# Performance work log

Measured on AMD Instinct MI355X. Metric: run time of the kernel, lower is better.

The kernel has to match this reference:

```python
import jax, jax.numpy as jnp
import numpy as np

INPUT_DIM = 512
MIX = 32
HID = 96
B, T = 256, 512


def setup_inputs() -> dict:
    key = jax.random.key(0)
    ks = jax.random.split(key, 8)
    s = lambda fan_in: 1.0 / np.sqrt(fan_in)
    x = jax.random.normal(ks[0], (B, T, INPUT_DIM), dtype=jnp.float32)
    # mix: Linear(INPUT_DIM, MIX, bias=False) -> weight [MIX, INPUT_DIM]
    W_mix = jax.random.uniform(ks[1], (MIX, INPUT_DIM), jnp.float32, -s(INPUT_DIM), s(INPUT_DIM))
    # GRU layer 0 weights, PyTorch layout: [3H, in], [3H, H], biases [3H]
    W_ih = jax.random.uniform(ks[2], (3 * HID, MIX), jnp.float32, -s(HID), s(HID))
    W_hh = jax.random.uniform(ks[3], (3 * HID, HID), jnp.float32, -s(HID), s(HID))
    b_ih = jax.random.uniform(ks[4], (3 * HID,), jnp.float32, -s(HID), s(HID))
    b_hh = jax.random.uniform(ks[5], (3 * HID,), jnp.float32, -s(HID), s(HID))
    # head: Linear(HID, MIX)
    W_head = jax.random.uniform(ks[6], (MIX, HID), jnp.float32, -s(HID), s(HID))
    b_head = jax.random.uniform(ks[7], (MIX,), jnp.float32, -s(HID), s(HID))
    return {"x": x, "W_mix": W_mix, "W_ih": W_ih, "W_hh": W_hh,
            "b_ih": b_ih, "b_hh": b_hh, "W_head": W_head, "b_head": b_head}


def _gru_last(z, W_ih, W_hh, b_ih, b_hh):
    # z: [B, T, MIX]. Precompute all input-side gate pre-activations: [T, B, 3H]
    gx = jnp.einsum('btm,gm->tbg', z, W_ih) + b_ih
    h0 = jnp.zeros((z.shape[0], HID), dtype=z.dtype)

    def step(h, gx_t):
        gh = h @ W_hh.T + b_hh  # [B, 3H]
        xr, xz, xn = jnp.split(gx_t, 3, axis=-1)
        hr, hz, hn = jnp.split(gh, 3, axis=-1)
        r = jax.nn.sigmoid(xr + hr)
        u = jax.nn.sigmoid(xz + hz)
        n = jnp.tanh(xn + r * hn)
        h_new = (1.0 - u) * n + u * h
        return h_new, None

    h_last, _ = jax.lax.scan(step, h0, gx)
    return h_last  # [B, HID]


def reference(x, W_mix, W_ih, W_hh, b_ih, b_hh, W_head, b_head):
    z = x @ W_mix.T                       # [B, T, MIX]
    last = _gru_last(z, W_ih, W_hh, b_ih, b_hh)  # [B, HID]
    z_next = last @ W_head.T + b_head     # [B, MIX]
    y_next = z_next @ W_mix               # [B, INPUT_DIM] (tied weights)
    return y_next
```

## Files before the change

### kernel.cpp

```cpp
#include <hip/hip_runtime.h>

#define IDIM 512
#define MIXD 32
#define HID 96
#define BB 256
#define TT 512
#define TROWS 32
#define SROW 516

typedef float f32x2 __attribute__((ext_vector_type(2)));
typedef float f32x4 __attribute__((ext_vector_type(4)));

#define EXP2(x) __builtin_amdgcn_exp2f(x)

template <int CTRL>
__device__ __forceinline__ float dpp_shl_add(float x) {
    int m = __builtin_amdgcn_update_dpp(0, __float_as_int(x), CTRL, 0xf, 0xf, true);
    return x + __int_as_float(m);
}
__device__ __forceinline__ float octet_reduce_lane0(float x) {
    x = dpp_shl_add<0x104>(x);
    x = dpp_shl_add<0x102>(x);
    x = dpp_shl_add<0x101>(x);
    return x;
}
__device__ __forceinline__ float red16(float x) {
    x = dpp_shl_add<0x108>(x);
    x = dpp_shl_add<0x104>(x);
    x = dpp_shl_add<0x102>(x);
    x = dpp_shl_add<0x101>(x);
    return x;
}
__device__ __forceinline__ f32x2 pkfma(f32x2 a, f32x2 b, f32x2 c) {
    asm("v_pk_fma_f32 %0, %1, %2, %0" : "+v"(c) : "v"(a), "v"(b));
    return c;
}

__global__ __launch_bounds__(256) void k_mix(const float* __restrict__ x,
                                             const float* __restrict__ Wmix,
                                             float* __restrict__ z) {
    __shared__ __align__(16) float sx[TROWS * SROW];
    const int tid = threadIdx.x;
    const int mg = (tid >> 4) & 7, ks = tid & 15, rr = tid >> 7;

    f32x2 w[4][16];
    #pragma unroll
    for (int mm = 0; mm < 4; ++mm) {
        #pragma unroll
        for (int i = 0; i < 8; ++i) {
            const int cj = (i + ks) & 7;
            f32x4 v = *(const f32x4*)(Wmix + (size_t)(4 * mg + mm) * IDIM + ks * 32 + cj * 4);
            w[mm][2*i] = v.xy; w[mm][2*i+1] = v.zw;
        }
    }

    const size_t rowbase = (size_t)blockIdx.x * 256;
    const float* xb = x + rowbase * IDIM;

    f32x4 st[16];
    #pragma unroll
    for (int i = 0; i < 16; ++i)
        st[i] = *(const f32x4*)(xb + (size_t)(tid + 256 * i) * 4);

    for (int t = 0; t < 8; ++t) {
        #pragma unroll
        for (int i = 0; i < 16; ++i) {
            const int v = tid + 256 * i, r = v >> 7, c = v & 127;
            *(f32x4*)(&sx[r * SROW + c * 4]) = st[i];
        }
        __syncthreads();

        if (t + 1 < 8) {
            const float* xn = xb + (size_t)(t + 1) * TROWS * IDIM;
            #pragma unroll
            for (int i = 0; i < 16; ++i)
                st[i] = *(const f32x4*)(xn + (size_t)(tid + 256 * i) * 4);
        }

        float* zp = z + (rowbase + (size_t)t * TROWS) * MIXD + 4 * mg;
        for (int rl = 0; rl < 16; ++rl) {
            const int r = rr * 16 + rl;
            const float* rp = sx + r * SROW + ks * 32;
            f32x2 a0 = {0.f,0.f}, a1 = {0.f,0.f}, a2 = {0.f,0.f}, a3 = {0.f,0.f};
            #pragma unroll
            for (int i = 0; i < 8; ++i) {
                f32x4 v = *(const f32x4*)(rp + ((i + ks) & 7) * 4);
                a0 = pkfma(w[0][2*i], v.xy, a0); a0 = pkfma(w[0][2*i+1], v.zw, a0);
                a1 = pkfma(w[1][2*i], v.xy, a1); a1 = pkfma(w[1][2*i+1], v.zw, a1);
                a2 = pkfma(w[2][2*i], v.xy, a2); a2 = pkfma(w[2][2*i+1], v.zw, a2);
                a3 = pkfma(w[3][2*i], v.xy, a3); a3 = pkfma(w[3][2*i+1], v.zw, a3);
            }
            float s0 = red16(a0.x + a0.y);
            float s1 = red16(a1.x + a1.y);
            float s2 = red16(a2.x + a2.y);
            float s3 = red16(a3.x + a3.y);
            if (ks == 0) {
                f32x4 o4 = { s0, s1, s2, s3 };
                *(f32x4*)(zp + (size_t)r * MIXD) = o4;
            }
        }
        __syncthreads();
    }
}

__global__ __launch_bounds__(256, 1) void k_scan(const float* __restrict__ z,
                                                 const float* __restrict__ Wih,
                                                 const float* __restrict__ Whh,
                                                 const float* __restrict__ bih,
                                                 const float* __restrict__ bhh,
                                                 const float* __restrict__ Whead,
                                                 const float* __restrict__ bhead,
                                                 const float* __restrict__ Wmix,
                                                 float* __restrict__ y) {
    const int b   = blockIdx.x;
    const int tid = threadIdx.x;
    const int j0  = tid >> 3;
    const int o   = tid & 7;
    const float L  = 1.4426950408889634f;
    const float L2 = 2.8853900817779268f;

    __shared__ __align__(16) float sz[256 * MIXD];
    __shared__ __align__(16) float shp[2][HID];
    __shared__ __align__(16) float szn[MIXD];

    f32x2 whr[3][6], whu[3][6], whn[3][6], wir[3][2], wiu[3][2], win[3][2];
    float br[3], bu[3], bxn[3], bhn[3];
    #pragma unroll
    for (int i = 0; i < 3; ++i) {
        const int j = j0 + 32 * i;
        #pragma unroll
        for (int c = 0; c < 3; ++c) {
            f32x4 v = *(const f32x4*)(Whh + (size_t)(j        ) * HID + o * 12 + c * 4);
            v *= L;  whr[i][2*c] = v.xy; whr[i][2*c+1] = v.zw;
        }
        #pragma unroll
        for (int c = 0; c < 3; ++c) {
            f32x4 v = *(const f32x4*)(Whh + (size_t)(j +   HID) * HID + o * 12 + c * 4);
            v *= L;  whu[i][2*c] = v.xy; whu[i][2*c+1] = v.zw;
        }
        #pragma unroll
        for (int c = 0; c < 3; ++c) {
            f32x4 v = *(const f32x4*)(Whh + (size_t)(j + 2*HID) * HID + o * 12 + c * 4);
            v *= L2; whn[i][2*c] = v.xy; whn[i][2*c+1] = v.zw;
        }
        {
            f32x4 v = *(const f32x4*)(Wih + (size_t)(j        ) * MIXD + o * 4);
            v *= L;  wir[i][0] = v.xy; wir[i][1] = v.zw;
        }
        {
            f32x4 v = *(const f32x4*)(Wih + (size_t)(j +   HID) * MIXD + o * 4);
            v *= L;  wiu[i][0] = v.xy; wiu[i][1] = v.zw;
        }
        {
            f32x4 v = *(const f32x4*)(Wih + (size_t)(j + 2*HID) * MIXD + o * 4);
            v *= L2; win[i][0] = v.xy; win[i][1] = v.zw;
        }
        br[i]  = (o == 0) ? L  * (bih[j]       + bhh[j])       : 0.f;
        bu[i]  = (o == 0) ? L  * (bih[j + HID] + bhh[j + HID]) : 0.f;
        bxn[i] = (o == 0) ? L2 * bih[j + 2*HID] : 0.f;
        bhn[i] = (o == 0) ? L2 * bhh[j + 2*HID] : 0.f;
    }

    float hown[3] = {0.f, 0.f, 0.f};
    if (tid < HID) shp[0][tid] = 0.f;

    const f32x4* zb4 = (const f32x4*)(z + (size_t)b * TT * MIXD);
    f32x4* sz4 = (f32x4*)sz;

    for (int c = 0; c < TT / 256; ++c) {
        #pragma unroll
        for (int i = 0; i < 8; ++i)
            sz4[tid + 256 * i] = zb4[c * 2048 + tid + 256 * i];
        __syncthreads();

        for (int tt = 0; tt < 256; ++tt) {
            const int t = (c << 8) + tt;
            const float* hr = shp[t & 1];
            float*       hw = shp[(t + 1) & 1];

            const f32x4 z4 = *(const f32x4*)(sz + tt * MIXD + o * 4);
            const f32x4 h0 = *(const f32x4*)(hr + o * 12);
            const f32x4 h1 = *(const f32x4*)(hr + o * 12 + 4);
            const f32x4 h2 = *(const f32x4*)(hr + o * 12 + 8);
            const f32x2 hh[6] = { h0.xy, h0.zw, h1.xy, h1.zw, h2.xy, h2.zw };

            float hv[3];
            #pragma unroll
            for (int i = 0; i < 3; ++i) {
                f32x2 aR  = {br[i],  0.f}, aU  = {bu[i],  0.f};
                f32x2 aXN = {bxn[i], 0.f}, aHN = {bhn[i], 0.f};

                aR  = __builtin_elementwise_fma(wir[i][0], z4.xy, aR);
                aR  = __builtin_elementwise_fma(wir[i][1], z4.zw, aR);
                aU  = __builtin_elementwise_fma(wiu[i][0], z4.xy, aU);
                aU  = __builtin_elementwise_fma(wiu[i][1], z4.zw, aU);
                aXN = __builtin_elementwise_fma(win[i][0], z4.xy, aXN);
                aXN = __builtin_elementwise_fma(win[i][1], z4.zw, aXN);

                #pragma unroll
                for (int k = 0; k < 6; ++k) {
                    aR  = __builtin_elementwise_fma(whr[i][k], hh[k], aR);
                    aU  = __builtin_elementwise_fma(whu[i][k], hh[k], aU);
                    aHN = __builtin_elementwise_fma(whn[i][k], hh[k], aHN);
                }

                float sR  = octet_reduce_lane0(aR.x  + aR.y);
                float sU  = octet_reduce_lane0(aU.x  + aU.y);
                float sXN = octet_reduce_lane0(aXN.x + aXN.y);
                float sHN = octet_reduce_lane0(aHN.x + aHN.y);

                float r = __builtin_amdgcn_rcpf(1.f + EXP2(-sR));
                float u = __builtin_amdgcn_rcpf(1.f + EXP2(-sU));
                float n = 1.f - 2.f * __builtin_amdgcn_rcpf(1.f + EXP2(sXN + r * sHN));
                hv[i] = u * (hown[i] - n) + n;
                hown[i] = hv[i];
            }
            if (o == 0) {
                hw[j0]      = hv[0];
                hw[j0 + 32] = hv[1];
                hw[j0 + 64] = hv[2];
            }
            __syncthreads();
        }
    }

    if (tid < MIXD) {
        const float* h = shp[0];
        float a0 = 0.f, a1 = 0.f, a2 = 0.f, a3 = 0.f;
        #pragma unroll
        for (int kc = 0; kc < HID / 4; ++kc) {
            f32x4 wv = *(const f32x4*)(Whead + (size_t)tid * HID + kc * 4);
            f32x4 hv4 = *(const f32x4*)(h + kc * 4);
            a0 += wv.x * hv4.x; a1 += wv.y * hv4.y;
            a2 += wv.z * hv4.z; a3 += wv.w * hv4.w;
        }
        szn[tid] = bhead[tid] + ((a0 + a1) + (a2 + a3));
    }
    __syncthreads();
    #pragma unroll
    for (int rep = 0; rep < 2; ++rep) {
        const int col = tid + 256 * rep;
        float acc = 0.f;
        #pragma unroll
        for (int m = 0; m < MIXD; ++m)
            acc += szn[m] * Wmix[(size_t)m * IDIM + col];
        y[(size_t)b * IDIM + col] = acc;
    }
}

extern "C" void kernel_launch(void* const* d_in, const int* in_sizes, int n_in,
                              void* d_out, int out_size, void* d_ws, size_t ws_size,
                              hipStream_t stream) {
    const float* x     = (const float*)d_in[0];
    const float* Wmix  = (const float*)d_in[1];
    const float* Wih   = (const float*)d_in[2];
    const float* Whh   = (const float*)d_in[3];
    const float* bih   = (const float*)d_in[4];
    const float* bhh   = (const float*)d_in[5];
    const float* Whead = (const float*)d_in[6];
    const float* bhead = (const float*)d_in[7];
    float* out = (float*)d_out;

    float* z = (float*)d_ws;

    k_mix <<<512, 256, 0, stream>>>(x, Wmix, z);
    k_scan<<<BB,  256, 0, stream>>>(z, Wih, Whh, bih, bhh, Whead, bhead, Wmix, out);
}
```

Before: 328.7 us.

## Pack two batch sequences per block in the GRU scan kernel

The scan kernel now runs 512-thread blocks, with each 256-thread half handling its own batch row. The grid is halved to 128 blocks, and shared buffers for z, the hidden state and the head output are duplicated per half. The aim is to interleave two independent recurrences on one CU so each hides the other's per-step latency. In exchange, both sequences share every block-wide barrier and only half as many CUs are busy. The 512-thread launch bound may also tighten the register budget for the large per-thread weight cache and cause spills.

```diff
diff --git a/kernel.cpp b/kernel.cpp
--- a/kernel.cpp
+++ b/kernel.cpp
@@ -103,7 +103,7 @@
     }
 }
 
-__global__ __launch_bounds__(256, 1) void k_scan(const float* __restrict__ z,
+__global__ __launch_bounds__(512, 1) void k_scan(const float* __restrict__ z,
                                                  const float* __restrict__ Wih,
                                                  const float* __restrict__ Whh,
                                                  const float* __restrict__ bih,
@@ -112,16 +112,18 @@
                                                  const float* __restrict__ bhead,
                                                  const float* __restrict__ Wmix,
                                                  float* __restrict__ y) {
-    const int b   = blockIdx.x;
-    const int tid = threadIdx.x;
-    const int j0  = tid >> 3;
-    const int o   = tid & 7;
+    const int tid  = threadIdx.x;
+    const int half = tid >> 8;
+    const int t2   = tid & 255;
+    const int b    = blockIdx.x * 2 + half;
+    const int j0   = t2 >> 3;
+    const int o    = t2 & 7;
     const float L  = 1.4426950408889634f;
     const float L2 = 2.8853900817779268f;
 
-    __shared__ __align__(16) float sz[256 * MIXD];
-    __shared__ __align__(16) float shp[2][HID];
-    __shared__ __align__(16) float szn[MIXD];
+    __shared__ __align__(16) float sz[2][256 * MIXD];
+    __shared__ __align__(16) float shp[2][2][HID];
+    __shared__ __align__(16) float szn[2][MIXD];
 
     f32x2 whr[3][6], whu[3][6], whn[3][6], wir[3][2], wiu[3][2], win[3][2];
     float br[3], bu[3], bxn[3], bhn[3];
@@ -162,23 +164,23 @@
     }
 
     float hown[3] = {0.f, 0.f, 0.f};
-    if (tid < HID) shp[0][tid] = 0.f;
+    if (t2 < HID) shp[half][0][t2] = 0.f;
 
     const f32x4* zb4 = (const f32x4*)(z + (size_t)b * TT * MIXD);
-    f32x4* sz4 = (f32x4*)sz;
+    f32x4* sz4 = (f32x4*)sz[half];
 
     for (int c = 0; c < TT / 256; ++c) {
         #pragma unroll
         for (int i = 0; i < 8; ++i)
-            sz4[tid + 256 * i] = zb4[c * 2048 + tid + 256 * i];
+            sz4[t2 + 256 * i] = zb4[c * 2048 + t2 + 256 * i];
         __syncthreads();
 
         for (int tt = 0; tt < 256; ++tt) {
             const int t = (c << 8) + tt;
-            const float* hr = shp[t & 1];
-            float*       hw = shp[(t + 1) & 1];
-
-            const f32x4 z4 = *(const f32x4*)(sz + tt * MIXD + o * 4);
+            const float* hr = shp[half][t & 1];
+            float*       hw = shp[half][(t + 1) & 1];
+
+            const f32x4 z4 = *(const f32x4*)(sz[half] + tt * MIXD + o * 4);
             const f32x4 h0 = *(const f32x4*)(hr + o * 12);
             const f32x4 h1 = *(const f32x4*)(hr + o * 12 + 4);
             const f32x4 h2 = *(const f32x4*)(hr + o * 12 + 8);
@@ -224,26 +226,26 @@
         }
     }
 
-    if (tid < MIXD) {
-        const float* h = shp[0];
+    if (t2 < MIXD) {
+        const float* h = shp[half][0];
         float a0 = 0.f, a1 = 0.f, a2 = 0.f, a3 = 0.f;
         #pragma unroll
         for (int kc = 0; kc < HID / 4; ++kc) {
-            f32x4 wv = *(const f32x4*)(Whead + (size_t)tid * HID + kc * 4);
+            f32x4 wv = *(const f32x4*)(Whead + (size_t)t2 * HID + kc * 4);
             f32x4 hv4 = *(const f32x4*)(h + kc * 4);
             a0 += wv.x * hv4.x; a1 += wv.y * hv4.y;
             a2 += wv.z * hv4.z; a3 += wv.w * hv4.w;
         }
-        szn[tid] = bhead[tid] + ((a0 + a1) + (a2 + a3));
+        szn[half][t2] = bhead[t2] + ((a0 + a1) + (a2 + a3));
     }
     __syncthreads();
     #pragma unroll
     for (int rep = 0; rep < 2; ++rep) {
-        const int col = tid + 256 * rep;
+        const int col = t2 + 256 * rep;
         float acc = 0.f;
         #pragma unroll
         for (int m = 0; m < MIXD; ++m)
-            acc += szn[m] * Wmix[(size_t)m * IDIM + col];
+            acc += szn[half][m] * Wmix[(size_t)m * IDIM + col];
         y[(size_t)b * IDIM + col] = acc;
     }
 }
@@ -264,5 +266,5 @@
     float* z = (float*)d_ws;
 
     k_mix <<<512, 256, 0, stream>>>(x, Wmix, z);
-    k_scan<<<BB,  256, 0, stream>>>(z, Wih, Whh, bih, bhh, Whead, bhead, Wmix, out);
-}
+    k_scan<<<BB / 2, 512, 0, stream>>>(z, Wih, Whh, bih, bhh, Whead, bhead, Wmix, out);
+}
```

Result: slower. 492.3 us (+49.8%).
